# Optimization experiments

Hardware: AMD Instinct MI355X
Metric: run time of the kernel (lower is better)

Reference implementation:

```python
import jax, jax.numpy as jnp
import numpy as np

D_OUT, D_IN = 4096, 11008
REMAINED = 5504            # int(D_IN * 0.5)
N_CLUSTERS = 64


def setup_inputs() -> dict:
    key = jax.random.key(0)
    k1, k2, k3, k4 = jax.random.split(key, 4)
    x = jax.random.normal(k1, (1, REMAINED), dtype=jnp.float32)
    weight = jax.random.normal(k2, (D_OUT, D_IN), dtype=jnp.float32) * 0.02
    bias = jax.random.normal(k3, (D_OUT,), dtype=jnp.float32) * 0.02
    act_idx = jax.random.randint(k4, (N_CLUSTERS, REMAINED), 0, D_IN, dtype=jnp.int64)
    return {"x": x, "weight": weight, "bias": bias, "act_idx": act_idx, "cluster": 3}


def reference(x, weight, bias, act_idx, cluster):
    # Decode (batch=1) path of ReduceLayer_fc2:
    # gather the activated columns for this cluster, then GEMV + bias.
    cols = act_idx[cluster]                 # [R] indices into d_in
    filtered_w = weight[:, cols]            # [D_out, R] column gather
    return x @ filtered_w.T + bias          # [1, D_out]
```

## Files before the change

### kernel.cpp

```cpp
#include <hip/hip_runtime.h>

constexpr int D_OUT    = 4096;
constexpr int D_IN     = 11008;
constexpr int REMAINED = 5504;
constexpr int NV       = D_IN / 4;
constexpr int BLK      = 256;
constexpr int ROWS     = 4;

__global__ __launch_bounds__(BLK) void scatter_kernel(
    const float* __restrict__ x,
    const int*   __restrict__ act_idx,
    const int*   __restrict__ cluster,
    float*       __restrict__ xd)
{
    int i = blockIdx.x * BLK + threadIdx.x;
    if (i < REMAINED) {
        int c   = cluster[0];
        int col = act_idx[(size_t)c * REMAINED + i];
        atomicAdd(xd + col, x[i]);
    }
}

__global__ __launch_bounds__(BLK) void gemv_kernel(
    const float4* __restrict__ W,
    const float4* __restrict__ xd,
    const float*  __restrict__ bias,
    float*        __restrict__ out)
{
    const int row0 = blockIdx.x * ROWS;
    const int tid  = threadIdx.x;
    const float4* w0 = W + (size_t)row0 * NV;

    float acc[ROWS] = {0.f, 0.f, 0.f, 0.f};
    for (int k = tid; k < NV; k += BLK) {
        float4 xv = xd[k];
        #pragma unroll
        for (int r = 0; r < ROWS; ++r) {
            float4 w = w0[(size_t)r * NV + k];
            acc[r] += w.x * xv.x + w.y * xv.y + w.z * xv.z + w.w * xv.w;
        }
    }

    __shared__ float red[ROWS][BLK / 64];
    const int lane = tid & 63;
    const int wave = tid >> 6;
    #pragma unroll
    for (int r = 0; r < ROWS; ++r) {
        float v = acc[r];
        #pragma unroll
        for (int off = 32; off > 0; off >>= 1)
            v += __shfl_down(v, off, 64);
        if (lane == 0) red[r][wave] = v;
    }
    __syncthreads();
    if (tid < ROWS) {
        float s = red[tid][0] + red[tid][1] + red[tid][2] + red[tid][3];
        out[row0 + tid] = s + bias[row0 + tid];
    }
}

extern "C" void kernel_launch(void* const* d_in, const int* in_sizes, int n_in,
                              void* d_out, int out_size, void* d_ws, size_t ws_size,
                              hipStream_t stream)
{
    const float* x       = (const float*)d_in[0];
    const float* weight  = (const float*)d_in[1];
    const float* bias    = (const float*)d_in[2];
    const int*   act_idx = (const int*)d_in[3];
    const int*   cluster = (const int*)d_in[4];
    float*       out     = (float*)d_out;
    float*       xd      = (float*)d_ws;

    hipMemsetAsync(xd, 0, D_IN * sizeof(float), stream);
    scatter_kernel<<<(REMAINED + BLK - 1) / BLK, BLK, 0, stream>>>(x, act_idx, cluster, xd);
    gemv_kernel<<<D_OUT / ROWS, BLK, 0, stream>>>(
        (const float4*)weight, (const float4*)xd, bias, out);
}
```

Before: 266.4 us.

## Fuse scatter into GEMV with per-block shared-memory x and nontemporal weight loads

Drops the memset and the separate global-atomic scatter kernel. Each GEMV block now zeroes a dense 11008-float x vector in shared memory and builds it with LDS atomics. Rows per block rise from 4 to 8, weight reads use nontemporal loads, and the dot product uses explicit fmaf chains. This removes two launches and a global round trip for the scatter. In exchange every block repeats the scatter work, and the roughly 44KB of LDS per block, with only 512 blocks, may limit occupancy for a bandwidth-bound GEMV.

```diff
diff --git a/kernel.cpp b/kernel.cpp
--- a/kernel.cpp
+++ b/kernel.cpp
@@ -5,43 +5,48 @@
 constexpr int REMAINED = 5504;
 constexpr int NV       = D_IN / 4;
 constexpr int BLK      = 256;
-constexpr int ROWS     = 4;
+constexpr int ROWS     = 8;
 
-__global__ __launch_bounds__(BLK) void scatter_kernel(
+typedef float fvec4 __attribute__((ext_vector_type(4)));
+
+__global__ __launch_bounds__(BLK) void fused_gemv_kernel(
     const float* __restrict__ x,
+    const fvec4* __restrict__ W,
+    const float* __restrict__ bias,
     const int*   __restrict__ act_idx,
     const int*   __restrict__ cluster,
-    float*       __restrict__ xd)
+    float*       __restrict__ out)
 {
-    int i = blockIdx.x * BLK + threadIdx.x;
-    if (i < REMAINED) {
-        int c   = cluster[0];
-        int col = act_idx[(size_t)c * REMAINED + i];
-        atomicAdd(xd + col, x[i]);
-    }
-}
+    __shared__ float xd[D_IN];
+    __shared__ float red[ROWS][BLK / 64];
 
-__global__ __launch_bounds__(BLK) void gemv_kernel(
-    const float4* __restrict__ W,
-    const float4* __restrict__ xd,
-    const float*  __restrict__ bias,
-    float*        __restrict__ out)
-{
+    const int tid = threadIdx.x;
+
+    #pragma unroll
+    for (int i = tid; i < D_IN; i += BLK) xd[i] = 0.f;
+    __syncthreads();
+
+    const int  c   = cluster[0];
+    const int* idx = act_idx + (size_t)c * REMAINED;
+    for (int i = tid; i < REMAINED; i += BLK)
+        atomicAdd(&xd[idx[i]], x[i]);
+    __syncthreads();
+
     const int row0 = blockIdx.x * ROWS;
-    const int tid  = threadIdx.x;
-    const float4* w0 = W + (size_t)row0 * NV;
+    const fvec4* w0  = W + (size_t)row0 * NV;
+    const fvec4* xd4 = (const fvec4*)xd;
 
-    float acc[ROWS] = {0.f, 0.f, 0.f, 0.f};
+    float acc[ROWS] = {};
     for (int k = tid; k < NV; k += BLK) {
-        float4 xv = xd[k];
+        fvec4 xv = xd4[k];
         #pragma unroll
         for (int r = 0; r < ROWS; ++r) {
-            float4 w = w0[(size_t)r * NV + k];
-            acc[r] += w.x * xv.x + w.y * xv.y + w.z * xv.z + w.w * xv.w;
+            fvec4 w = __builtin_nontemporal_load(&w0[(size_t)r * NV + k]);
+            acc[r] = fmaf(w.x, xv.x, fmaf(w.y, xv.y,
+                     fmaf(w.z, xv.z, fmaf(w.w, xv.w, acc[r]))));
         }
     }
 
-    __shared__ float red[ROWS][BLK / 64];
     const int lane = tid & 63;
     const int wave = tid >> 6;
     #pragma unroll
@@ -69,10 +74,7 @@
     const int*   act_idx = (const int*)d_in[3];
     const int*   cluster = (const int*)d_in[4];
     float*       out     = (float*)d_out;
-    float*       xd      = (float*)d_ws;
 
-    hipMemsetAsync(xd, 0, D_IN * sizeof(float), stream);
-    scatter_kernel<<<(REMAINED + BLK - 1) / BLK, BLK, 0, stream>>>(x, act_idx, cluster, xd);
-    gemv_kernel<<<D_OUT / ROWS, BLK, 0, stream>>>(
-        (const float4*)weight, (const float4*)xd, bias, out);
+    fused_gemv_kernel<<<D_OUT / ROWS, BLK, 0, stream>>>(
+        x, (const fvec4*)weight, bias, act_idx, cluster, out);
 }
```

Result: faster. 253.6 us (-4.8%).
